# Kernel optimization log

Hardware: AMD Instinct MI355X
Metric: run time of the kernel (lower is better)

The kernel has to match this reference:

```python
import jax, jax.numpy as jnp
import numpy as np

B, T, D = 2, 2048, 1024
H, KVH = 16, 4
HD = D // H            # 64
HALF = HD // 2         # 32
DFF = 4096
KW = 15
EPS = 1e-6


def zcrms(x, scale):
    # zero-centred RMSNorm: (1 + scale) * x / rms(x)
    rms = jnp.sqrt(jnp.mean(jnp.square(x.astype(jnp.float32)), axis=-1, keepdims=True) + EPS)
    return ((1.0 + scale) * x / rms).astype(x.dtype)


def apply_rope(x, cos, sin):
    # x: [B, H, T, HD]; cos/sin: [T, HALF]
    c = cos[None, None, :, :]
    s = sin[None, None, :, :]
    x1, x2 = x[..., :HALF], x[..., HALF:]
    return jnp.concatenate([x1 * c - x2 * s, x2 * c + x1 * s], axis=-1)


def setup_inputs() -> dict:
    key = jax.random.key(0)
    ks = jax.random.split(key, 20)
    std = 0.02
    inp = {
        "x": jax.random.normal(ks[0], (B, T, D), jnp.float32),
        "mask": jnp.ones((1, 1, T, T), dtype=bool),
        "cos": jnp.cos(jnp.arange(T, dtype=jnp.float32)[:, None]
                       * (10000.0 ** (-jnp.arange(HALF, dtype=jnp.float32) / HALF))[None, :]),
        "sin": jnp.sin(jnp.arange(T, dtype=jnp.float32)[:, None]
                       * (10000.0 ** (-jnp.arange(HALF, dtype=jnp.float32) / HALF))[None, :]),
        # attention
        "attn_norm_scale": jax.random.normal(ks[1], (D,), jnp.float32) * std,
        "q_kernel": jax.random.normal(ks[2], (D, D), jnp.float32) * std,
        "k_kernel": jax.random.normal(ks[3], (D, KVH * HD), jnp.float32) * std,
        "v_kernel": jax.random.normal(ks[4], (D, KVH * HD), jnp.float32) * std,
        "q_norm_scale": jax.random.normal(ks[5], (HD,), jnp.float32) * std,
        "k_norm_scale": jax.random.normal(ks[6], (HD,), jnp.float32) * std,
        "o_kernel": jax.random.normal(ks[7], (D, D), jnp.float32) * std,
        # conv module
        "conv_norm_scale": jax.random.normal(ks[8], (D,), jnp.float32) * std,
        "pw_up_kernel": jax.random.normal(ks[9], (D, 2 * D), jnp.float32) * std,
        "dw_kernel": jax.random.normal(ks[10], (KW, 1, D), jnp.float32) * std,
        "conv_inner_norm_scale": jax.random.normal(ks[11], (D,), jnp.float32) * std,
        "pw_down_kernel": jax.random.normal(ks[12], (D, D), jnp.float32) * std,
        # ffn
        "ffn_norm_scale": jax.random.normal(ks[13], (D,), jnp.float32) * std,
        "gate_kernel": jax.random.normal(ks[14], (D, DFF), jnp.float32) * std,
        "up_kernel": jax.random.normal(ks[15], (D, DFF), jnp.float32) * std,
        "down_kernel": jax.random.normal(ks[16], (DFF, D), jnp.float32) * std,
    }
    return inp


def reference(x, mask, cos, sin, attn_norm_scale, q_kernel, k_kernel, v_kernel,
              q_norm_scale, k_norm_scale, o_kernel, conv_norm_scale, pw_up_kernel,
              dw_kernel, conv_inner_norm_scale, pw_down_kernel, ffn_norm_scale,
              gate_kernel, up_kernel, down_kernel):
    # ---- pre-norm self-attention (GQA + QK-RMSNorm + RoPE) ----
    h = zcrms(x, attn_norm_scale)
    q = (h @ q_kernel).reshape(B, T, H, HD).transpose(0, 2, 1, 3)      # [B,H,T,HD]
    k = (h @ k_kernel).reshape(B, T, KVH, HD).transpose(0, 2, 1, 3)    # [B,KVH,T,HD]
    v = (h @ v_kernel).reshape(B, T, KVH, HD).transpose(0, 2, 1, 3)
    q = zcrms(q, q_norm_scale)
    k = zcrms(k, k_norm_scale)
    rep = H // KVH
    k = jnp.repeat(k, rep, axis=1)
    v = jnp.repeat(v, rep, axis=1)
    q = apply_rope(q, cos, sin)
    k = apply_rope(k, cos, sin)
    scale = jnp.sqrt(jnp.float32(HD))
    aw = jnp.einsum('bhqd,bhkd->bhqk', q, k) / scale
    aw = jnp.where(mask, aw, jnp.finfo(aw.dtype).min)
    aw = jax.nn.softmax(aw, axis=-1)
    attn = jnp.einsum('bhqk,bhkd->bhqd', aw, v).transpose(0, 2, 1, 3).reshape(B, T, D)
    x = x + attn @ o_kernel

    # ---- conformer conv module: pw_up -> GLU -> depthwise conv -> norm -> pw_down ----
    h = zcrms(x, conv_norm_scale)
    u = h @ pw_up_kernel
    u1, u2 = jnp.split(u, 2, axis=-1)
    g = u1 * jax.nn.sigmoid(u2)                                        # [B,T,D]
    c = jax.lax.conv_general_dilated(
        g, dw_kernel, window_strides=(1,), padding='SAME',
        feature_group_count=D, dimension_numbers=('NWC', 'WIO', 'NWC'))
    c = zcrms(c, conv_inner_norm_scale)
    x = x + c @ pw_down_kernel

    # ---- gated FFN with drelu activation ----
    h = zcrms(x, ffn_norm_scale)
    ff = jax.nn.relu(h @ gate_kernel) * jax.nn.relu(h @ up_kernel)
    x = x + ff @ down_kernel
    return x
```

## Files before the change

kernel.cpp:

```cpp
#include <hip/hip_runtime.h>


#define TT   2048
#define NTOK 4096

typedef __attribute__((ext_vector_type(8))) short short8;
typedef __attribute__((ext_vector_type(4))) float floatx4;

__device__ __forceinline__ unsigned short f2bf(float f) {
  unsigned int u = __float_as_uint(f);
  u = (u + 0x7fffu + ((u >> 16) & 1u)) >> 16;
  return (unsigned short)u;
}
__device__ __forceinline__ float bf2f(unsigned short s) {
  return __uint_as_float(((unsigned int)s) << 16);
}

__device__ __forceinline__ void glds16(const void* g, void* lds_base) {
  __builtin_amdgcn_global_load_lds(
      (const __attribute__((address_space(1))) void*)g,
      (__attribute__((address_space(3))) void*)lds_base, 16, 0, 0);
}

struct WJobs {
  const float* src[9];
  unsigned short* dst[9];
  int K[9], M[9];
  int start[10];
};

__global__ __launch_bounds__(256) void wconv_all_kernel(WJobs tab) {
  int b = blockIdx.x;
  int j = 0;
  while (b >= tab.start[j + 1]) j++;
  int t = b - tab.start[j];
  const float* src = tab.src[j];
  unsigned short* dst = tab.dst[j];
  int K = tab.K[j], M = tab.M[j];
  int mt = M >> 5;
  int m0 = (t % mt) * 32, k0 = (t / mt) * 32;
  __shared__ float tile[32][33];
  int tx = threadIdx.x & 31, ty = threadIdx.x >> 5;
  for (int r = ty; r < 32; r += 8)
    tile[r][tx] = src[(size_t)(k0 + r) * M + m0 + tx];
  __syncthreads();
  for (int r = ty; r < 32; r += 8)
    dst[(size_t)(m0 + r) * K + k0 + tx] = f2bf(tile[tx][r]);
}

__global__ __launch_bounds__(256) void rmsnorm_kernel(
    const float* __restrict__ x, const float* __restrict__ scale,
    unsigned short* __restrict__ out) {
  int t = blockIdx.x, tid = threadIdx.x;
  float4 xv = ((const float4*)(x + (size_t)t * 1024))[tid];
  float ss = xv.x * xv.x + xv.y * xv.y + xv.z * xv.z + xv.w * xv.w;
#pragma unroll
  for (int off = 32; off > 0; off >>= 1) ss += __shfl_down(ss, off);
  __shared__ float red[4];
  if ((tid & 63) == 0) red[tid >> 6] = ss;
  __syncthreads();
  float rinv = rsqrtf((red[0] + red[1] + red[2] + red[3]) * (1.0f / 1024.0f) + 1e-6f);
  float4 sv = ((const float4*)scale)[tid];
  ushort4 o;
  o.x = f2bf((1.0f + sv.x) * xv.x * rinv);
  o.y = f2bf((1.0f + sv.y) * xv.y * rinv);
  o.z = f2bf((1.0f + sv.z) * xv.z * rinv);
  o.w = f2bf((1.0f + sv.w) * xv.w * rinv);
  ((ushort4*)(out + (size_t)t * 1024))[tid] = o;
}

template <int BN, bool OUT_BF16, bool RELU, bool RESID>
__global__ __launch_bounds__(256, 2) void gemm_bt_kernel(
    const unsigned short* __restrict__ A, const unsigned short* __restrict__ Bt,
    void* __restrict__ Cout, const float* __restrict__ resid, int K, int M) {
  constexpr int NI = BN / 32;
  __shared__ __align__(16) unsigned short As[128 * 64];
  __shared__ __align__(16) unsigned short Bs[BN * 64];
  const int tid = threadIdx.x;
  const int wid = tid >> 6, lane = tid & 63;
  const int quad = lane >> 4, l16 = lane & 15;
  const int wm = (wid >> 1) * 64, wn = (wid & 1) * (BN / 2);
  const int row0 = blockIdx.y * 128;
  const int col0 = blockIdx.x * BN;

  floatx4 acc[4][NI];
#pragma unroll
  for (int mi = 0; mi < 4; mi++)
#pragma unroll
    for (int ni = 0; ni < NI; ni++) acc[mi][ni] = (floatx4){0.f, 0.f, 0.f, 0.f};

  const unsigned short* Ag = A + (size_t)row0 * K;
  const unsigned short* Bg = Bt + (size_t)col0 * K;

  for (int k0 = 0; k0 < K; k0 += 64) {
#pragma unroll
    for (int j = 0; j < 4; j++) {
      int ci = tid + j * 256;
      int r = ci >> 3, c = (ci & 7) ^ (r & 7);
      glds16(Ag + (size_t)r * K + k0 + c * 8, &As[(wid * 64 + j * 256) * 8]);
    }
#pragma unroll
    for (int j = 0; j < BN / 32; j++) {
      int ci = tid + j * 256;
      int r = ci >> 3, c = (ci & 7) ^ (r & 7);
      glds16(Bg + (size_t)r * K + k0 + c * 8, &Bs[(wid * 64 + j * 256) * 8]);
    }
    __syncthreads();
#pragma unroll
    for (int kk = 0; kk < 64; kk += 32) {
      short8 a[4], b[NI];
#pragma unroll
      for (int mi = 0; mi < 4; mi++) {
        int r = wm + mi * 16 + l16;
        a[mi] = *(const short8*)&As[r * 64 + (((kk >> 3) + quad) ^ (r & 7)) * 8];
      }
#pragma unroll
      for (int ni = 0; ni < NI; ni++) {
        int r = wn + ni * 16 + l16;
        b[ni] = *(const short8*)&Bs[r * 64 + (((kk >> 3) + quad) ^ (r & 7)) * 8];
      }
#pragma unroll
      for (int mi = 0; mi < 4; mi++)
#pragma unroll
        for (int ni = 0; ni < NI; ni++)
          acc[mi][ni] = __builtin_amdgcn_mfma_f32_16x16x32_bf16(a[mi], b[ni], acc[mi][ni], 0, 0, 0);
    }
    __syncthreads();
  }
#pragma unroll
  for (int mi = 0; mi < 4; mi++) {
#pragma unroll
    for (int reg = 0; reg < 4; reg++) {
      int grow = row0 + wm + mi * 16 + quad * 4 + reg;
#pragma unroll
      for (int ni = 0; ni < NI; ni++) {
        int gcol = col0 + wn + ni * 16 + l16;
        float v = acc[mi][ni][reg];
        if (RESID) v += resid[(size_t)grow * M + gcol];
        if (RELU) v = fmaxf(v, 0.f);
        if (OUT_BF16) ((unsigned short*)Cout)[(size_t)grow * M + gcol] = f2bf(v);
        else          ((float*)Cout)[(size_t)grow * M + gcol] = v;
      }
    }
  }
}

#define QSCALE 0.180336880111f

__global__ __launch_bounds__(256) void qknorm_rope_kernel(
    const float* __restrict__ qkv, const float* __restrict__ cosb,
    const float* __restrict__ sinb, const float* __restrict__ qns,
    const float* __restrict__ kns, unsigned short* __restrict__ qb,
    unsigned short* __restrict__ kb, unsigned short* __restrict__ vb) {
  int tok = blockIdx.x;
  int tid = threadIdx.x, w = tid >> 6, lane = tid & 63;
  int pos = tok & (TT - 1);
  int half = lane & 31;
  float c = cosb[pos * 32 + half], s = sinb[pos * 32 + half];
  const float* row = qkv + (size_t)tok * 1536;
  for (int hr = w; hr < 20; hr += 4) {
    float v = row[hr * 64 + lane];
    float ss = v * v;
#pragma unroll
    for (int off = 32; off > 0; off >>= 1) ss += __shfl_xor(ss, off);
    float rinv = rsqrtf(ss * (1.0f / 64.0f) + 1e-6f);
    float sc = (hr < 16) ? qns[lane] : kns[lane];
    float nv = (1.0f + sc) * v * rinv;
    float partner = __shfl_xor(nv, 32);
    float outv = (lane < 32) ? (nv * c - partner * s) : (nv * c + partner * s);
    if (hr < 16) qb[(size_t)tok * 1024 + hr * 64 + lane] = f2bf(outv * QSCALE);
    else         kb[(size_t)tok * 256 + (hr - 16) * 64 + lane] = f2bf(outv);
  }
  vb[(size_t)tok * 256 + tid] = f2bf(row[1280 + tid]);
}

__global__ __launch_bounds__(256) void vtrans_kernel(
    const unsigned short* __restrict__ vb, unsigned short* __restrict__ vt) {
  __shared__ unsigned short t[64 * 65];
  int ktile = blockIdx.x;
  int g = blockIdx.y;
  int bi = g >> 2, kvh = g & 3;
  int tid = threadIdx.x;
#pragma unroll
  for (int j = 0; j < 2; j++) {
    int ci = tid + j * 256;
    int r = ci >> 3, c8 = (ci & 7) * 8;
    union { uint4 v; unsigned short u[8]; } uu;
    uu.v = *(const uint4*)(vb + (size_t)(bi * TT + ktile * 64 + r) * 256 + kvh * 64 + c8);
#pragma unroll
    for (int e = 0; e < 8; e++) t[r * 65 + c8 + e] = uu.u[e];
  }
  __syncthreads();
#pragma unroll
  for (int j = 0; j < 2; j++) {
    int ci = tid + j * 256;
    int d = ci >> 3, c8 = (ci & 7) * 8;
    union { uint4 v; unsigned short u[8]; } uu;
#pragma unroll
    for (int e = 0; e < 8; e++) uu.u[e] = t[(c8 + e) * 65 + d];
    *(uint4*)(vt + ((size_t)(g * 64 + d)) * TT + ktile * 64 + c8) = uu.v;
  }
}

__global__ __launch_bounds__(256) void flash_kernel(
    const unsigned short* __restrict__ qb, const unsigned short* __restrict__ kb,
    const unsigned short* __restrict__ vt, unsigned short* __restrict__ ob) {
  const int qt = blockIdx.x;
  const int bh = blockIdx.y;
  const int bi = bh >> 4, h = bh & 15, kvh = h >> 2;
  const int tid = threadIdx.x, w = tid >> 6, lane = tid & 63;
  const int quad = lane >> 4, l16 = lane & 15;

  __shared__ __align__(16) unsigned short Ks[2][64 * 64];
  __shared__ __align__(16) unsigned short Vs[2][64 * 64];
  __shared__ __align__(16) unsigned short Ps[128 * 72];

  const unsigned short* qsrc = qb + ((size_t)(bi * TT + qt * 128)) * 1024 + h * 64;
  short8 qf[2][2];
#pragma unroll
  for (int af = 0; af < 2; af++) {
    const unsigned short* qr = qsrc + (size_t)(w * 32 + af * 16 + l16) * 1024;
    qf[af][0] = *(const short8*)(qr + quad * 8);
    qf[af][1] = *(const short8*)(qr + 32 + quad * 8);
  }

  const unsigned short* kbase = kb + ((size_t)(bi * TT)) * 256 + kvh * 64;
  const unsigned short* vbase = vt + ((size_t)(bi * 4 + kvh)) * (64 * TT);

  floatx4 oacc[2][4];
  floatx4 lacc[2];
#pragma unroll
  for (int af = 0; af < 2; af++) {
    lacc[af] = (floatx4){0.f, 0.f, 0.f, 0.f};
#pragma unroll
    for (int di = 0; di < 4; di++) oacc[af][di] = (floatx4){0.f, 0.f, 0.f, 0.f};
  }
  const short8 ones = (short8){0x3F80, 0x3F80, 0x3F80, 0x3F80,
                               0x3F80, 0x3F80, 0x3F80, 0x3F80};

#pragma unroll
  for (int j = 0; j < 2; j++) {
    int ci = tid + j * 256;
    int r = ci >> 3, c = (ci & 7) ^ (r & 7);
    glds16(kbase + (size_t)r * 256 + c * 8, &Ks[0][(w * 64 + j * 256) * 8]);
    glds16(vbase + (size_t)r * TT + c * 8, &Vs[0][(w * 64 + j * 256) * 8]);
  }

  for (int kt = 0; kt < 32; kt++) {
    const int buf = kt & 1;
    __syncthreads();
    if (kt < 31) {
#pragma unroll
      for (int j = 0; j < 2; j++) {
        int ci = tid + j * 256;
        int r = ci >> 3, c = (ci & 7) ^ (r & 7);
        glds16(kbase + (size_t)((kt + 1) * 64 + r) * 256 + c * 8,
               &Ks[buf ^ 1][(w * 64 + j * 256) * 8]);
        glds16(vbase + (size_t)r * TT + (kt + 1) * 64 + c * 8,
               &Vs[buf ^ 1][(w * 64 + j * 256) * 8]);
      }
    }

    short8 kf[4][2];
#pragma unroll
    for (int ni = 0; ni < 4; ni++) {
      int rb = ni * 16 + l16;
      kf[ni][0] = *(const short8*)&Ks[buf][rb * 64 + ((quad ^ (rb & 7)) * 8)];
      kf[ni][1] = *(const short8*)&Ks[buf][rb * 64 + (((4 + quad) ^ (rb & 7)) * 8)];
    }
#pragma unroll
    for (int af = 0; af < 2; af++) {
#pragma unroll
      for (int ni = 0; ni < 4; ni++) {
        floatx4 s = (floatx4){0.f, 0.f, 0.f, 0.f};
        s = __builtin_amdgcn_mfma_f32_16x16x32_bf16(qf[af][0], kf[ni][0], s, 0, 0, 0);
        s = __builtin_amdgcn_mfma_f32_16x16x32_bf16(qf[af][1], kf[ni][1], s, 0, 0, 0);
#pragma unroll
        for (int r = 0; r < 4; r++)
          Ps[(w * 32 + af * 16 + quad * 4 + r) * 72 + ((ni ^ quad) * 16 + l16)] =
              (unsigned short)(__float_as_uint(__builtin_amdgcn_exp2f(s[r])) >> 16);
      }
    }
    short8 vf[4][2];
#pragma unroll
    for (int di = 0; di < 4; di++) {
      int rb = di * 16 + l16;
      vf[di][0] = *(const short8*)&Vs[buf][rb * 64 + ((quad ^ (rb & 7)) * 8)];
      vf[di][1] = *(const short8*)&Vs[buf][rb * 64 + (((4 + quad) ^ (rb & 7)) * 8)];
    }
#pragma unroll
    for (int af = 0; af < 2; af++) {
      const int rr = w * 32 + af * 16 + l16;
      const int sw = l16 >> 2;
      short8 pa0 = *(const short8*)&Ps[rr * 72 + (((quad >> 1) ^ sw) * 16 + (quad & 1) * 8)];
      short8 pa1 = *(const short8*)&Ps[rr * 72 + ((((quad >> 1) + 2) ^ sw) * 16 + (quad & 1) * 8)];
      lacc[af] = __builtin_amdgcn_mfma_f32_16x16x32_bf16(pa0, ones, lacc[af], 0, 0, 0);
      lacc[af] = __builtin_amdgcn_mfma_f32_16x16x32_bf16(pa1, ones, lacc[af], 0, 0, 0);
#pragma unroll
      for (int di = 0; di < 4; di++) {
        oacc[af][di] = __builtin_amdgcn_mfma_f32_16x16x32_bf16(pa0, vf[di][0], oacc[af][di], 0, 0, 0);
        oacc[af][di] = __builtin_amdgcn_mfma_f32_16x16x32_bf16(pa1, vf[di][1], oacc[af][di], 0, 0, 0);
      }
    }
  }

  unsigned short* obase = ob + ((size_t)(bi * TT + qt * 128)) * 1024 + h * 64;
#pragma unroll
  for (int af = 0; af < 2; af++) {
    float rl[4];
#pragma unroll
    for (int r = 0; r < 4; r++) rl[r] = 1.0f / lacc[af][r];
#pragma unroll
    for (int di = 0; di < 4; di++)
#pragma unroll
      for (int r = 0; r < 4; r++) {
        int qrow = w * 32 + af * 16 + quad * 4 + r;
        obase[(size_t)qrow * 1024 + di * 16 + l16] = f2bf(oacc[af][di][r] * rl[r]);
      }
  }
}

__global__ __launch_bounds__(256) void glu_kernel(const float* __restrict__ u,
                                                  unsigned short* __restrict__ g) {
  int idx = blockIdx.x * 256 + threadIdx.x;
  int t = idx >> 8, c4 = (idx & 255) * 4;
  float4 a = *(const float4*)(u + (size_t)t * 2048 + c4);
  float4 b = *(const float4*)(u + (size_t)t * 2048 + 1024 + c4);
  ushort4 o;
  o.x = f2bf(a.x / (1.0f + __expf(-b.x)));
  o.y = f2bf(a.y / (1.0f + __expf(-b.y)));
  o.z = f2bf(a.z / (1.0f + __expf(-b.z)));
  o.w = f2bf(a.w / (1.0f + __expf(-b.w)));
  *(ushort4*)(g + (size_t)t * 1024 + c4) = o;
}

__global__ __launch_bounds__(256) void convnorm_kernel(
    const unsigned short* __restrict__ g, const float* __restrict__ dw,
    const float* __restrict__ scale, unsigned short* __restrict__ out) {
  int tok = blockIdx.x;
  int bi = tok >> 11, pos = tok & (TT - 1);
  int tid = threadIdx.x, c0 = tid * 4;
  float a0 = 0.f, a1 = 0.f, a2 = 0.f, a3 = 0.f;
#pragma unroll
  for (int wk = 0; wk < 15; wk++) {
    int pp = pos + wk - 7;
    if (pp < 0 || pp >= TT) continue;
    ushort4 gv = *(const ushort4*)(g + ((size_t)(bi * TT + pp)) * 1024 + c0);
    float4 kv = *(const float4*)(dw + wk * 1024 + c0);
    a0 += bf2f(gv.x) * kv.x;
    a1 += bf2f(gv.y) * kv.y;
    a2 += bf2f(gv.z) * kv.z;
    a3 += bf2f(gv.w) * kv.w;
  }
  float ss = a0 * a0 + a1 * a1 + a2 * a2 + a3 * a3;
#pragma unroll
  for (int off = 32; off > 0; off >>= 1) ss += __shfl_down(ss, off);
  __shared__ float red[4];
  if ((tid & 63) == 0) red[tid >> 6] = ss;
  __syncthreads();
  float rinv = rsqrtf((red[0] + red[1] + red[2] + red[3]) * (1.0f / 1024.0f) + 1e-6f);
  float4 sv = *(const float4*)(scale + c0);
  ushort4 o;
  o.x = f2bf((1.0f + sv.x) * a0 * rinv);
  o.y = f2bf((1.0f + sv.y) * a1 * rinv);
  o.z = f2bf((1.0f + sv.z) * a2 * rinv);
  o.w = f2bf((1.0f + sv.w) * a3 * rinv);
  *(ushort4*)(out + (size_t)tok * 1024 + c0) = o;
}

__global__ __launch_bounds__(256) void ffmul_kernel(
    const unsigned short* __restrict__ gu, unsigned short* __restrict__ ff) {
  int idx = blockIdx.x * 256 + threadIdx.x;
  int t = idx >> 10, c4 = (idx & 1023) * 4;
  ushort4 a = *(const ushort4*)(gu + (size_t)t * 8192 + c4);
  ushort4 b = *(const ushort4*)(gu + (size_t)t * 8192 + 4096 + c4);
  ushort4 o;
  o.x = f2bf(bf2f(a.x) * bf2f(b.x));
  o.y = f2bf(bf2f(a.y) * bf2f(b.y));
  o.z = f2bf(bf2f(a.z) * bf2f(b.z));
  o.w = f2bf(bf2f(a.w) * bf2f(b.w));
  *(ushort4*)(ff + (size_t)t * 4096 + c4) = o;
}

extern "C" void kernel_launch(void* const* d_in, const int* in_sizes, int n_in,
                              void* d_out, int out_size, void* d_ws, size_t ws_size,
                              hipStream_t stream) {
  const float* x        = (const float*)d_in[0];
  const float* cosb     = (const float*)d_in[2];
  const float* sinb     = (const float*)d_in[3];
  const float* attn_ns  = (const float*)d_in[4];
  const float* qkern    = (const float*)d_in[5];
  const float* kkern    = (const float*)d_in[6];
  const float* vkern    = (const float*)d_in[7];
  const float* qns      = (const float*)d_in[8];
  const float* kns      = (const float*)d_in[9];
  const float* okern    = (const float*)d_in[10];
  const float* conv_ns  = (const float*)d_in[11];
  const float* pwupk    = (const float*)d_in[12];
  const float* dwk      = (const float*)d_in[13];
  const float* convi_ns = (const float*)d_in[14];
  const float* pwdnk    = (const float*)d_in[15];
  const float* ffn_ns   = (const float*)d_in[16];
  const float* gatek    = (const float*)d_in[17];
  const float* upk      = (const float*)d_in[18];
  const float* downk    = (const float*)d_in[19];
  float* out = (float*)d_out;
  char* ws = (char*)d_ws;

  const size_t O_QKVT = 0;
  const size_t O_OT   = O_QKVT + (size_t)1536 * 1024 * 2;
  const size_t O_UPT  = O_OT   + (size_t)1024 * 1024 * 2;
  const size_t O_DNT  = O_UPT  + (size_t)2048 * 1024 * 2;
  const size_t O_GUT  = O_DNT  + (size_t)1024 * 1024 * 2;
  const size_t O_DWNT = O_GUT  + (size_t)8192 * 1024 * 2;
  const size_t O_H    = O_DWNT + (size_t)4096 * 1024 * 2;
  const size_t O_BIG1 = O_H    + (size_t)4096 * 1024 * 2;
  const size_t O_QB   = O_BIG1 + (size_t)4096 * 8192 * 2;
  const size_t O_KB   = O_QB   + (size_t)4096 * 1024 * 2;
  const size_t O_VB   = O_KB   + (size_t)4096 * 256 * 2;
  const size_t O_VT   = O_VB   + (size_t)4096 * 256 * 2;
  const size_t O_ECN  = O_VT   + (size_t)8 * 64 * 2048 * 2;
  const size_t O_X1   = O_ECN  + (size_t)4096 * 1024 * 2;
  const size_t O_X2   = O_X1   + (size_t)4096 * 1024 * 4;
  const size_t O_BIG2 = O_X2   + (size_t)4096 * 1024 * 4;

  unsigned short* qkvT = (unsigned short*)(ws + O_QKVT);
  unsigned short* oT   = (unsigned short*)(ws + O_OT);
  unsigned short* upT  = (unsigned short*)(ws + O_UPT);
  unsigned short* dnT  = (unsigned short*)(ws + O_DNT);
  unsigned short* guT  = (unsigned short*)(ws + O_GUT);
  unsigned short* dwT  = (unsigned short*)(ws + O_DWNT);
  unsigned short* hbuf = (unsigned short*)(ws + O_H);
  float*          big1f = (float*)(ws + O_BIG1);
  unsigned short* big1u = (unsigned short*)(ws + O_BIG1);
  unsigned short* qbuf = (unsigned short*)(ws + O_QB);
  unsigned short* kbuf = (unsigned short*)(ws + O_KB);
  unsigned short* vbuf = (unsigned short*)(ws + O_VB);
  unsigned short* vtb  = (unsigned short*)(ws + O_VT);
  unsigned short* ecn  = (unsigned short*)(ws + O_ECN);
  float*          x1   = (float*)(ws + O_X1);
  float*          x2   = (float*)(ws + O_X2);
  unsigned short* big2 = (unsigned short*)(ws + O_BIG2);

  WJobs tab;
  tab.src[0] = qkern;  tab.dst[0] = qkvT;                         tab.K[0] = 1024; tab.M[0] = 1024;
  tab.src[1] = kkern;  tab.dst[1] = qkvT + (size_t)1024 * 1024;   tab.K[1] = 1024; tab.M[1] = 256;
  tab.src[2] = vkern;  tab.dst[2] = qkvT + (size_t)1280 * 1024;   tab.K[2] = 1024; tab.M[2] = 256;
  tab.src[3] = okern;  tab.dst[3] = oT;                           tab.K[3] = 1024; tab.M[3] = 1024;
  tab.src[4] = pwupk;  tab.dst[4] = upT;                          tab.K[4] = 1024; tab.M[4] = 2048;
  tab.src[5] = pwdnk;  tab.dst[5] = dnT;                          tab.K[5] = 1024; tab.M[5] = 1024;
  tab.src[6] = gatek;  tab.dst[6] = guT;                          tab.K[6] = 1024; tab.M[6] = 4096;
  tab.src[7] = upk;    tab.dst[7] = guT + (size_t)4096 * 1024;    tab.K[7] = 1024; tab.M[7] = 4096;
  tab.src[8] = downk;  tab.dst[8] = dwT;                          tab.K[8] = 4096; tab.M[8] = 1024;
  tab.start[0] = 0;
  for (int i = 0; i < 9; i++)
    tab.start[i + 1] = tab.start[i] + (tab.M[i] >> 5) * (tab.K[i] >> 5);
  wconv_all_kernel<<<tab.start[9], 256, 0, stream>>>(tab);

  rmsnorm_kernel<<<NTOK, 256, 0, stream>>>(x, attn_ns, hbuf);
  gemm_bt_kernel<128, false, false, false><<<dim3(12, 32), 256, 0, stream>>>(
      hbuf, qkvT, big1f, nullptr, 1024, 1536);
  qknorm_rope_kernel<<<NTOK, 256, 0, stream>>>(big1f, cosb, sinb, qns, kns,
                                               qbuf, kbuf, vbuf);
  vtrans_kernel<<<dim3(32, 8), 256, 0, stream>>>(vbuf, vtb);
  flash_kernel<<<dim3(16, 32), 256, 0, stream>>>(qbuf, kbuf, vtb, ecn);
  gemm_bt_kernel<64, false, false, true><<<dim3(16, 32), 256, 0, stream>>>(
      ecn, oT, x1, x, 1024, 1024);

  rmsnorm_kernel<<<NTOK, 256, 0, stream>>>(x1, conv_ns, hbuf);
  gemm_bt_kernel<128, false, false, false><<<dim3(16, 32), 256, 0, stream>>>(
      hbuf, upT, big1f, nullptr, 1024, 2048);
  glu_kernel<<<4096, 256, 0, stream>>>(big1f, big2);
  convnorm_kernel<<<NTOK, 256, 0, stream>>>(big2, dwk, convi_ns, ecn);
  gemm_bt_kernel<64, false, false, true><<<dim3(16, 32), 256, 0, stream>>>(
      ecn, dnT, x2, x1, 1024, 1024);

  rmsnorm_kernel<<<NTOK, 256, 0, stream>>>(x2, ffn_ns, hbuf);
  gemm_bt_kernel<128, true, true, false><<<dim3(64, 32), 256, 0, stream>>>(
      hbuf, guT, big1u, nullptr, 1024, 8192);
  ffmul_kernel<<<16384, 256, 0, stream>>>(big1u, big2);
  gemm_bt_kernel<64, false, false, true><<<dim3(16, 32), 256, 0, stream>>>(
      big2, dwT, out, x2, 4096, 1024);
}
```

Measured before the change: 516.4 us.

## Fuse GLU and drelu products into GEMM epilogues via interleaved weight layout

Weight conversion now interleaves gate/up (and GLU halves) in 32-row groups so each GEMM tile holds matching pairs of columns. The GEMM epilogue then computes sigmoid-gated GLU or relu*relu directly and writes a half-width bf16 output. This removes the separate glu and ffmul kernels and their round trips through large intermediates. The QKV projection also writes bf16 instead of fp32, which halves that traffic but adds a rounding step before the q/k norm.

Result: faster. 484.9 us (-6.1%).

```diff
diff --git a/kernel.cpp b/kernel.cpp
--- a/kernel.cpp
+++ b/kernel.cpp
@@ -25,7 +25,7 @@
 struct WJobs {
   const float* src[9];
   unsigned short* dst[9];
-  int K[9], M[9];
+  int K[9], M[9], pm[9];
   int start[10];
 };
 
@@ -36,16 +36,21 @@
   int t = b - tab.start[j];
   const float* src = tab.src[j];
   unsigned short* dst = tab.dst[j];
-  int K = tab.K[j], M = tab.M[j];
+  int K = tab.K[j], M = tab.M[j], pm = tab.pm[j];
   int mt = M >> 5;
   int m0 = (t % mt) * 32, k0 = (t / mt) * 32;
+  int rowbase;
+  if (pm == 0)      rowbase = m0;
+  else if (pm == 1) rowbase = ((m0 & 1023) >> 5) * 64 + (m0 >> 10) * 32;
+  else if (pm == 2) rowbase = (m0 >> 5) * 64;
+  else              rowbase = (m0 >> 5) * 64 + 32;
   __shared__ float tile[32][33];
   int tx = threadIdx.x & 31, ty = threadIdx.x >> 5;
   for (int r = ty; r < 32; r += 8)
     tile[r][tx] = src[(size_t)(k0 + r) * M + m0 + tx];
   __syncthreads();
   for (int r = ty; r < 32; r += 8)
-    dst[(size_t)(m0 + r) * K + k0 + tx] = f2bf(tile[tx][r]);
+    dst[(size_t)(rowbase + r) * K + k0 + tx] = f2bf(tile[tx][r]);
 }
 
 __global__ __launch_bounds__(256) void rmsnorm_kernel(
@@ -69,7 +74,7 @@
   ((ushort4*)(out + (size_t)t * 1024))[tid] = o;
 }
 
-template <int BN, bool OUT_BF16, bool RELU, bool RESID>
+template <int BN, int FUSE, bool OUT_BF16, bool RELU, bool RESID>
 __global__ __launch_bounds__(256, 2) void gemm_bt_kernel(
     const unsigned short* __restrict__ A, const unsigned short* __restrict__ Bt,
     void* __restrict__ Cout, const float* __restrict__ resid, int K, int M) {
@@ -127,19 +132,41 @@
     }
     __syncthreads();
   }
-#pragma unroll
-  for (int mi = 0; mi < 4; mi++) {
-#pragma unroll
-    for (int reg = 0; reg < 4; reg++) {
-      int grow = row0 + wm + mi * 16 + quad * 4 + reg;
-#pragma unroll
-      for (int ni = 0; ni < NI; ni++) {
-        int gcol = col0 + wn + ni * 16 + l16;
-        float v = acc[mi][ni][reg];
-        if (RESID) v += resid[(size_t)grow * M + gcol];
-        if (RELU) v = fmaxf(v, 0.f);
-        if (OUT_BF16) ((unsigned short*)Cout)[(size_t)grow * M + gcol] = f2bf(v);
-        else          ((float*)Cout)[(size_t)grow * M + gcol] = v;
+
+  if (FUSE == 0) {
+#pragma unroll
+    for (int mi = 0; mi < 4; mi++) {
+#pragma unroll
+      for (int reg = 0; reg < 4; reg++) {
+        int grow = row0 + wm + mi * 16 + quad * 4 + reg;
+#pragma unroll
+        for (int ni = 0; ni < NI; ni++) {
+          int gcol = col0 + wn + ni * 16 + l16;
+          float v = acc[mi][ni][reg];
+          if (RESID) v += resid[(size_t)grow * M + gcol];
+          if (RELU) v = fmaxf(v, 0.f);
+          if (OUT_BF16) ((unsigned short*)Cout)[(size_t)grow * M + gcol] = f2bf(v);
+          else          ((float*)Cout)[(size_t)grow * M + gcol] = v;
+        }
+      }
+    }
+  } else {
+    const int group = (col0 + wn) >> 6;
+    const int MW = M >> 1;
+#pragma unroll
+    for (int mi = 0; mi < 4; mi++) {
+#pragma unroll
+      for (int reg = 0; reg < 4; reg++) {
+        int grow = row0 + wm + mi * 16 + quad * 4 + reg;
+#pragma unroll
+        for (int ni = 0; ni < NI / 2; ni++) {
+          int f = group * 32 + ni * 16 + l16;
+          float a = acc[mi][ni][reg], b = acc[mi][ni + NI / 2][reg];
+          float v;
+          if (FUSE == 1) v = a / (1.0f + __expf(-b));
+          else           v = fmaxf(a, 0.f) * fmaxf(b, 0.f);
+          ((unsigned short*)Cout)[(size_t)grow * MW + f] = f2bf(v);
+        }
       }
     }
   }
@@ -148,7 +175,7 @@
 #define QSCALE 0.180336880111f
 
 __global__ __launch_bounds__(256) void qknorm_rope_kernel(
-    const float* __restrict__ qkv, const float* __restrict__ cosb,
+    const unsigned short* __restrict__ qkv, const float* __restrict__ cosb,
     const float* __restrict__ sinb, const float* __restrict__ qns,
     const float* __restrict__ kns, unsigned short* __restrict__ qb,
     unsigned short* __restrict__ kb, unsigned short* __restrict__ vb) {
@@ -157,9 +184,9 @@
   int pos = tok & (TT - 1);
   int half = lane & 31;
   float c = cosb[pos * 32 + half], s = sinb[pos * 32 + half];
-  const float* row = qkv + (size_t)tok * 1536;
+  const unsigned short* row = qkv + (size_t)tok * 1536;
   for (int hr = w; hr < 20; hr += 4) {
-    float v = row[hr * 64 + lane];
+    float v = bf2f(row[hr * 64 + lane]);
     float ss = v * v;
 #pragma unroll
     for (int off = 32; off > 0; off >>= 1) ss += __shfl_xor(ss, off);
@@ -171,7 +198,7 @@
     if (hr < 16) qb[(size_t)tok * 1024 + hr * 64 + lane] = f2bf(outv * QSCALE);
     else         kb[(size_t)tok * 256 + (hr - 16) * 64 + lane] = f2bf(outv);
   }
-  vb[(size_t)tok * 256 + tid] = f2bf(row[1280 + tid]);
+  vb[(size_t)tok * 256 + tid] = row[1280 + tid];
 }
 
 __global__ __launch_bounds__(256) void vtrans_kernel(
@@ -318,20 +345,6 @@
         obase[(size_t)qrow * 1024 + di * 16 + l16] = f2bf(oacc[af][di][r] * rl[r]);
       }
   }
-}
-
-__global__ __launch_bounds__(256) void glu_kernel(const float* __restrict__ u,
-                                                  unsigned short* __restrict__ g) {
-  int idx = blockIdx.x * 256 + threadIdx.x;
-  int t = idx >> 8, c4 = (idx & 255) * 4;
-  float4 a = *(const float4*)(u + (size_t)t * 2048 + c4);
-  float4 b = *(const float4*)(u + (size_t)t * 2048 + 1024 + c4);
-  ushort4 o;
-  o.x = f2bf(a.x / (1.0f + __expf(-b.x)));
-  o.y = f2bf(a.y / (1.0f + __expf(-b.y)));
-  o.z = f2bf(a.z / (1.0f + __expf(-b.z)));
-  o.w = f2bf(a.w / (1.0f + __expf(-b.w)));
-  *(ushort4*)(g + (size_t)t * 1024 + c4) = o;
 }
 
 __global__ __launch_bounds__(256) void convnorm_kernel(
@@ -366,20 +379,6 @@
   o.z = f2bf((1.0f + sv.z) * a2 * rinv);
   o.w = f2bf((1.0f + sv.w) * a3 * rinv);
   *(ushort4*)(out + (size_t)tok * 1024 + c0) = o;
-}
-
-__global__ __launch_bounds__(256) void ffmul_kernel(
-    const unsigned short* __restrict__ gu, unsigned short* __restrict__ ff) {
-  int idx = blockIdx.x * 256 + threadIdx.x;
-  int t = idx >> 10, c4 = (idx & 1023) * 4;
-  ushort4 a = *(const ushort4*)(gu + (size_t)t * 8192 + c4);
-  ushort4 b = *(const ushort4*)(gu + (size_t)t * 8192 + 4096 + c4);
-  ushort4 o;
-  o.x = f2bf(bf2f(a.x) * bf2f(b.x));
-  o.y = f2bf(bf2f(a.y) * bf2f(b.y));
-  o.z = f2bf(bf2f(a.z) * bf2f(b.z));
-  o.w = f2bf(bf2f(a.w) * bf2f(b.w));
-  *(ushort4*)(ff + (size_t)t * 4096 + c4) = o;
 }
 
 extern "C" void kernel_launch(void* const* d_in, const int* in_sizes, int n_in,
@@ -431,7 +430,6 @@
   unsigned short* guT  = (unsigned short*)(ws + O_GUT);
   unsigned short* dwT  = (unsigned short*)(ws + O_DWNT);
   unsigned short* hbuf = (unsigned short*)(ws + O_H);
-  float*          big1f = (float*)(ws + O_BIG1);
   unsigned short* big1u = (unsigned short*)(ws + O_BIG1);
   unsigned short* qbuf = (unsigned short*)(ws + O_QB);
   unsigned short* kbuf = (unsigned short*)(ws + O_KB);
@@ -443,42 +441,40 @@
   unsigned short* big2 = (unsigned short*)(ws + O_BIG2);
 
   WJobs tab;
-  tab.src[0] = qkern;  tab.dst[0] = qkvT;                         tab.K[0] = 1024; tab.M[0] = 1024;
-  tab.src[1] = kkern;  tab.dst[1] = qkvT + (size_t)1024 * 1024;   tab.K[1] = 1024; tab.M[1] = 256;
-  tab.src[2] = vkern;  tab.dst[2] = qkvT + (size_t)1280 * 1024;   tab.K[2] = 1024; tab.M[2] = 256;
-  tab.src[3] = okern;  tab.dst[3] = oT;                           tab.K[3] = 1024; tab.M[3] = 1024;
-  tab.src[4] = pwupk;  tab.dst[4] = upT;                          tab.K[4] = 1024; tab.M[4] = 2048;
-  tab.src[5] = pwdnk;  tab.dst[5] = dnT;                          tab.K[5] = 1024; tab.M[5] = 1024;
-  tab.src[6] = gatek;  tab.dst[6] = guT;                          tab.K[6] = 1024; tab.M[6] = 4096;
-  tab.src[7] = upk;    tab.dst[7] = guT + (size_t)4096 * 1024;    tab.K[7] = 1024; tab.M[7] = 4096;
-  tab.src[8] = downk;  tab.dst[8] = dwT;                          tab.K[8] = 4096; tab.M[8] = 1024;
+  tab.src[0] = qkern;  tab.dst[0] = qkvT;                       tab.K[0] = 1024; tab.M[0] = 1024; tab.pm[0] = 0;
+  tab.src[1] = kkern;  tab.dst[1] = qkvT + (size_t)1024 * 1024; tab.K[1] = 1024; tab.M[1] = 256;  tab.pm[1] = 0;
+  tab.src[2] = vkern;  tab.dst[2] = qkvT + (size_t)1280 * 1024; tab.K[2] = 1024; tab.M[2] = 256;  tab.pm[2] = 0;
+  tab.src[3] = okern;  tab.dst[3] = oT;                         tab.K[3] = 1024; tab.M[3] = 1024; tab.pm[3] = 0;
+  tab.src[4] = pwupk;  tab.dst[4] = upT;                        tab.K[4] = 1024; tab.M[4] = 2048; tab.pm[4] = 1;
+  tab.src[5] = pwdnk;  tab.dst[5] = dnT;                        tab.K[5] = 1024; tab.M[5] = 1024; tab.pm[5] = 0;
+  tab.src[6] = gatek;  tab.dst[6] = guT;                        tab.K[6] = 1024; tab.M[6] = 4096; tab.pm[6] = 2;
+  tab.src[7] = upk;    tab.dst[7] = guT;                        tab.K[7] = 1024; tab.M[7] = 4096; tab.pm[7] = 3;
+  tab.src[8] = downk;  tab.dst[8] = dwT;                        tab.K[8] = 4096; tab.M[8] = 1024; tab.pm[8] = 0;
   tab.start[0] = 0;
   for (int i = 0; i < 9; i++)
     tab.start[i + 1] = tab.start[i] + (tab.M[i] >> 5) * (tab.K[i] >> 5);
   wconv_all_kernel<<<tab.start[9], 256, 0, stream>>>(tab);
 
   rmsnorm_kernel<<<NTOK, 256, 0, stream>>>(x, attn_ns, hbuf);
-  gemm_bt_kernel<128, false, false, false><<<dim3(12, 32), 256, 0, stream>>>(
-      hbuf, qkvT, big1f, nullptr, 1024, 1536);
-  qknorm_rope_kernel<<<NTOK, 256, 0, stream>>>(big1f, cosb, sinb, qns, kns,
+  gemm_bt_kernel<128, 0, true, false, false><<<dim3(12, 32), 256, 0, stream>>>(
+      hbuf, qkvT, big1u, nullptr, 1024, 1536);
+  qknorm_rope_kernel<<<NTOK, 256, 0, stream>>>(big1u, cosb, sinb, qns, kns,
                                                qbuf, kbuf, vbuf);
   vtrans_kernel<<<dim3(32, 8), 256, 0, stream>>>(vbuf, vtb);
   flash_kernel<<<dim3(16, 32), 256, 0, stream>>>(qbuf, kbuf, vtb, ecn);
-  gemm_bt_kernel<64, false, false, true><<<dim3(16, 32), 256, 0, stream>>>(
+  gemm_bt_kernel<64, 0, false, false, true><<<dim3(16, 32), 256, 0, stream>>>(
       ecn, oT, x1, x, 1024, 1024);
 
   rmsnorm_kernel<<<NTOK, 256, 0, stream>>>(x1, conv_ns, hbuf);
-  gemm_bt_kernel<128, false, false, false><<<dim3(16, 32), 256, 0, stream>>>(
-      hbuf, upT, big1f, nullptr, 1024, 2048);
-  glu_kernel<<<4096, 256, 0, stream>>>(big1f, big2);
+  gemm_bt_kernel<128, 1, false, false, false><<<dim3(16, 32), 256, 0, stream>>>(
+      hbuf, upT, big2, nullptr, 1024, 2048);
   convnorm_kernel<<<NTOK, 256, 0, stream>>>(big2, dwk, convi_ns, ecn);
-  gemm_bt_kernel<64, false, false, true><<<dim3(16, 32), 256, 0, stream>>>(
+  gemm_bt_kernel<64, 0, false, false, true><<<dim3(16, 32), 256, 0, stream>>>(
       ecn, dnT, x2, x1, 1024, 1024);
 
   rmsnorm_kernel<<<NTOK, 256, 0, stream>>>(x2, ffn_ns, hbuf);
-  gemm_bt_kernel<128, true, true, false><<<dim3(64, 32), 256, 0, stream>>>(
+  gemm_bt_kernel<128, 2, false, false, false><<<dim3(64, 32), 256, 0, stream>>>(
       hbuf, guT, big1u, nullptr, 1024, 8192);
-  ffmul_kernel<<<16384, 256, 0, stream>>>(big1u, big2);
-  gemm_bt_kernel<64, false, false, true><<<dim3(16, 32), 256, 0, stream>>>(
-      big2, dwT, out, x2, 4096, 1024);
-}
+  gemm_bt_kernel<64, 0, false, false, true><<<dim3(16, 32), 256, 0, stream>>>(
+      big1u, dwT, out, x2, 4096, 1024);
+}
```
